# Kernel tuning notes

Measured on AMD Instinct MI355X. Metric: run time of the kernel, lower is better.

Reference implementation:

```python
import jax, jax.numpy as jnp
import numpy as np

ALPHA, GAMMA, EPS, BIG = 0.25, 2.0, 1e-7, 1e7
STRIDES = (8, 16, 32, 64, 128)
SHRINK = 0.2


def _project(boxes, fw, fh, stride):
    # shrink box around its center by SHRINK, project to feature grid (floor/ceil), clip
    cx = (boxes[..., 0] + boxes[..., 2]) * 0.5
    cy = (boxes[..., 1] + boxes[..., 3]) * 0.5
    hw = (boxes[..., 2] - boxes[..., 0]) * 0.5 * SHRINK
    hh = (boxes[..., 3] - boxes[..., 1]) * 0.5 * SHRINK
    x1 = jnp.clip(jnp.floor((cx - hw) / stride).astype(jnp.int32), 0, fw - 1)
    y1 = jnp.clip(jnp.floor((cy - hh) / stride).astype(jnp.int32), 0, fh - 1)
    x2 = jnp.clip(jnp.ceil((cx + hw) / stride).astype(jnp.int32), 1, fw)
    y2 = jnp.clip(jnp.ceil((cy + hh) / stride).astype(jnp.int32), 1, fh)
    return x1, y1, x2, y2


def _level_loss(cls_l, regr_l, boxes, labels, stride, fh, fw):
    # cls_l [B,fh,fw,C], regr_l [B,fh,fw,4], boxes [B,G,4], labels [B,G] -> loss [B,G]
    B, G = labels.shape
    x1, y1, x2, y2 = _project(boxes, fw, fh, stride)
    xs = jnp.arange(fw, dtype=jnp.int32)
    ys = jnp.arange(fh, dtype=jnp.int32)
    mx = (xs[None, None] >= x1[..., None]) & (xs[None, None] < x2[..., None])  # [B,G,fw]
    my = (ys[None, None] >= y1[..., None]) & (ys[None, None] < y2[..., None])  # [B,G,fh]
    mask = my[..., :, None] & mx[..., None, :]                                 # [B,G,fh,fw]
    denom = jnp.maximum(jnp.sum(mask, axis=(2, 3)).astype(cls_l.dtype), 1.0)   # = #positives

    # focal over one-hot(gt_label): sum_c = f0 - neg[gt] + pos[gt]
    p = jnp.clip(cls_l, EPS, 1.0 - EPS)
    neg = (1.0 - ALPHA) * p ** GAMMA * (-jnp.log1p(-p))   # per-class label=0 term
    pos = ALPHA * (1.0 - p) ** GAMMA * (-jnp.log(p))      # per-class label=1 term
    f0 = jnp.sum(neg, axis=-1)                            # [B,fh,fw]
    bidx = jnp.arange(B)[:, None]
    neg_g = neg[bidx, :, :, labels]                       # [B,G,fh,fw]
    pos_g = pos[bidx, :, :, labels]                       # [B,G,fh,fw]
    focal_map = f0[:, None] - neg_g + pos_g
    loss_cls = jnp.sum(jnp.where(mask, focal_map, 0.0), axis=(2, 3)) / denom

    # iou loss on (l,t,r,b)/(4*stride) targets, mean over region
    sx = (xs.astype(cls_l.dtype) + 0.5) * stride          # [fw]
    sy = (ys.astype(cls_l.dtype) + 0.5) * stride          # [fh]
    s = 1.0 / (4.0 * stride)
    tl = jnp.maximum(sx[None, None, None] - boxes[..., 0, None, None], 0.0) * s    # [B,G,1,fw]
    tt = jnp.maximum(sy[None, None, :, None] - boxes[..., 1, None, None], 0.0) * s  # [B,G,fh,1]
    tr = jnp.maximum(boxes[..., 2, None, None] - sx[None, None, None], 0.0) * s     # [B,G,1,fw]
    tb = jnp.maximum(boxes[..., 3, None, None] - sy[None, None, :, None], 0.0) * s  # [B,G,fh,1]
    pl = regr_l[..., 0][:, None]   # [B,1,fh,fw]
    pt = regr_l[..., 1][:, None]
    pr = regr_l[..., 2][:, None]
    pb = regr_l[..., 3][:, None]
    t_area = (tl + tr) * (tt + tb)                        # [B,G,fh,fw]
    p_area = (pl + pr) * (pt + pb)                        # [B,1,fh,fw]
    w_i = jnp.minimum(pl, tl) + jnp.minimum(pr, tr)
    h_i = jnp.minimum(pb, tb) + jnp.minimum(pt, tt)
    a_i = w_i * h_i
    a_u = t_area + p_area - a_i
    iou_map = -jnp.log((a_i + EPS) / (a_u + EPS))
    loss_iou = jnp.sum(jnp.where(mask, iou_map, 0.0), axis=(2, 3)) / denom

    empty = (x1 == x2) | (y1 == y2)                       # tf.cond 'do_not_match' branch
    return jnp.where(empty, BIG, loss_cls + loss_iou)


def _all_level_losses(cls_pred, regr_pred, gt_boxes, feature_shapes):
    fs = np.asarray(feature_shapes)
    B, C = cls_pred.shape[0], cls_pred.shape[-1]
    labels = jnp.clip(gt_boxes[..., 4].astype(jnp.int32), 0, C - 1)
    boxes = gt_boxes[..., :4]
    losses, start = [], 0
    for i, stride in enumerate(STRIDES):
        fh, fw = int(fs[i, 0]), int(fs[i, 1])
        cls_l = cls_pred[:, start:start + fh * fw].reshape(B, fh, fw, C)
        regr_l = regr_pred[:, start:start + fh * fw].reshape(B, fh, fw, 4)
        losses.append(_level_loss(cls_l, regr_l, boxes, labels, float(stride), fh, fw))
        start += fh * fw
    return jnp.stack(losses, axis=-1)   # [B,G,L]


def setup_inputs():
    key = jax.random.key(0)
    k = jax.random.split(key, 7)
    B, G, C = 8, 64, 80
    feature_shapes = np.array([[128, 128], [64, 64], [32, 32], [16, 16], [8, 8]], dtype=np.int32)
    total = int(np.prod(feature_shapes, axis=-1).sum())   # 21824 locations (1024x1024 img)
    cls_pred = jax.random.uniform(k[0], (B, total, C), jnp.float32, 0.01, 0.99)
    regr_pred = jax.random.uniform(k[1], (B, total, 4), jnp.float32, 0.05, 2.0)
    cx = jax.random.uniform(k[2], (B, G), jnp.float32, 64.0, 960.0)
    cy = jax.random.uniform(k[3], (B, G), jnp.float32, 64.0, 960.0)
    w = jax.random.uniform(k[4], (B, G), jnp.float32, 32.0, 320.0)
    h = jax.random.uniform(k[5], (B, G), jnp.float32, 32.0, 320.0)
    x1 = jnp.clip(cx - w / 2, 0.0, 1024.0)
    y1 = jnp.clip(cy - h / 2, 0.0, 1024.0)
    x2 = jnp.clip(cx + w / 2, 0.0, 1024.0)
    y2 = jnp.clip(cy + h / 2, 0.0, 1024.0)
    lbl = jax.random.randint(k[6], (B, G), 0, C).astype(jnp.float32)
    gt_boxes = jnp.stack([x1, y1, x2, y2, lbl], axis=-1)
    keep = (jnp.arange(G) < G - 16).astype(jnp.float32)   # last 16 rows are zero padding
    gt_boxes = gt_boxes * keep[None, :, None]
    return {"cls_pred": cls_pred, "regr_pred": regr_pred,
            "feature_shapes": feature_shapes, "gt_boxes": gt_boxes}


def reference(cls_pred, regr_pred, feature_shapes, gt_boxes):
    losses = _all_level_losses(cls_pred, regr_pred, gt_boxes, feature_shapes)   # [B,G,L]
    levels = jnp.argmin(losses, axis=-1).astype(jnp.int32)                      # [B,G]
    valid = jnp.sum(jnp.abs(gt_boxes[..., :4]), axis=-1) > 0                    # trim_padding_boxes
    levels = jnp.where(valid, levels, -1)                                       # padded boxes -> -1
    return levels.reshape(-1)
```

## Files before the change

kernel.cpp:

```cpp
#include <hip/hip_runtime.h>
#include <math.h>

static constexpr int B = 8;
static constexpr int G = 64;
static constexpr int C = 80;
static constexpr int TOTAL = 21824;
static constexpr float EPSF = 1e-7f;
static constexpr float BIGF = 1e7f;

static constexpr int LOCS = 128;
static constexpr int PAD  = 84;

__device__ __forceinline__ double wave_sum_d(double v) {
#pragma unroll
    for (int off = 32; off > 0; off >>= 1)
        v += __shfl_xor(v, off, 64);
    return v;
}

__device__ __forceinline__ float neg_fast(float x) {
    float p = fminf(fmaxf(x, EPSF), 1.0f - EPSF);
    float nl = -__logf(1.0f - p);
    return 0.75f * p * p * nl;
}

__global__ __launch_bounds__(128) void f0_kernel(const float* __restrict__ cls,
                                                 float* __restrict__ f0) {
    __shared__ float lds[LOCS * PAD];
    const int t = (int)threadIdx.x;
    const size_t baseLoc = (size_t)blockIdx.x * LOCS;
    const float4* gsrc = (const float4*)(cls + baseLoc * C);

#pragma unroll
    for (int r = 0; r < 20; ++r) {
        int q = r * LOCS + t;
        float4 v = gsrc[q];
        int loc = q / 20, chunk = q - loc * 20;
        *(float4*)&lds[loc * PAD + chunk * 4] = v;
    }
    __syncthreads();

    double acc = 0.0;
    const float* row = &lds[t * PAD];
#pragma unroll
    for (int i = 0; i < 20; ++i) {
        float4 v = *(const float4*)&row[i * 4];
        acc += (double)neg_fast(v.x);
        acc += (double)neg_fast(v.y);
        acc += (double)neg_fast(v.z);
        acc += (double)neg_fast(v.w);
    }
    f0[baseLoc + t] = (float)acc;
}

__global__ __launch_bounds__(320) void select_kernel(
        const float* __restrict__ cls, const float* __restrict__ regr,
        const float* __restrict__ gt, const float* __restrict__ f0,
        int* __restrict__ out) {
    const int   fws[5]     = {128, 64, 32, 16, 8};
    const int   offs[5]    = {0, 16384, 20480, 21504, 21760};
    const float strides[5] = {8.f, 16.f, 32.f, 64.f, 128.f};

    __shared__ float lloss[5];
    const int boxid = (int)blockIdx.x;
    const int l     = (int)(threadIdx.x >> 6);
    const int lane  = (int)(threadIdx.x & 63);

    const float* box = gt + (size_t)boxid * 5;
    float b0 = box[0], b1 = box[1], b2 = box[2], b3 = box[3];
    if (fabsf(b0) + fabsf(b1) + fabsf(b2) + fabsf(b3) <= 0.0f) {
        if (threadIdx.x == 0) out[boxid] = -1;
        return;
    }
    int label = (int)box[4];
    label = min(max(label, 0), C - 1);
    int b = boxid / G;

    float cx = (b0 + b2) * 0.5f, cy = (b1 + b3) * 0.5f;
    float hw = (b2 - b0) * 0.5f * 0.2f, hh = (b3 - b1) * 0.5f * 0.2f;

    const float st = strides[l];
    const int fw = fws[l];
    int x1 = min(max((int)floorf((cx - hw) / st), 0), fw - 1);
    int y1 = min(max((int)floorf((cy - hh) / st), 0), fw - 1);
    int x2 = min(max((int)ceilf((cx + hw) / st), 1), fw);
    int y2 = min(max((int)ceilf((cy + hh) / st), 1), fw);

    float loss;
    if (x1 == x2 || y1 == y2) {
        loss = BIGF;
    } else {
        int rw = x2 - x1;
        int area = rw * (y2 - y1);
        double sf = 0.0, si = 0.0;
        float s = 1.0f / (4.0f * st);
        for (int idx = lane; idx < area; idx += 64) {
            int yy = y1 + idx / rw;
            int xx = x1 + idx % rw;
            int loc = offs[l] + yy * fw + xx;
            size_t base = (size_t)b * TOTAL + (size_t)loc;
            float pv = cls[base * C + label];
            float p = fminf(fmaxf(pv, EPSF), 1.0f - EPSF);
            float neg_g = 0.75f * p * p * (-log1pf(-p));
            float omp = 1.0f - p;
            float pos_g = 0.25f * omp * omp * (-logf(p));
            sf += (double)((f0[base] - neg_g) + pos_g);
            const float4 r = *(const float4*)(regr + base * 4);
            float sx = ((float)xx + 0.5f) * st;
            float sy = ((float)yy + 0.5f) * st;
            float tl = fmaxf(sx - b0, 0.0f) * s;
            float tt = fmaxf(sy - b1, 0.0f) * s;
            float tr = fmaxf(b2 - sx, 0.0f) * s;
            float tb = fmaxf(b3 - sy, 0.0f) * s;
            float t_area = (tl + tr) * (tt + tb);
            float p_area = (r.x + r.z) * (r.y + r.w);
            float w_i = fminf(r.x, tl) + fminf(r.z, tr);
            float h_i = fminf(r.w, tb) + fminf(r.y, tt);
            float a_i = w_i * h_i;
            float a_u = (t_area + p_area) - a_i;
            si += (double)(-logf((a_i + EPSF) / (a_u + EPSF)));
        }
        sf = wave_sum_d(sf);
        si = wave_sum_d(si);
        float denom = (float)area;
        loss = (float)sf / denom + (float)si / denom;
    }
    if (lane == 0) lloss[l] = loss;
    __syncthreads();

    if (threadIdx.x == 0) {
        float best = lloss[0];
        int bestl = 0;
#pragma unroll
        for (int k = 1; k < 5; ++k) {
            float v = lloss[k];
            if (v < best) { best = v; bestl = k; }
        }
        out[boxid] = bestl;
    }
}

extern "C" void kernel_launch(void* const* d_in, const int* in_sizes, int n_in,
                              void* d_out, int out_size, void* d_ws, size_t ws_size,
                              hipStream_t stream) {
    const float* cls  = (const float*)d_in[0];
    const float* regr = (const float*)d_in[1];
    const float* gt   = (const float*)d_in[3];

    float* f0 = (float*)d_ws;

    f0_kernel<<<dim3((B * TOTAL) / LOCS), dim3(LOCS), 0, stream>>>(cls, f0);

    select_kernel<<<dim3(B * G), dim3(320), 0, stream>>>(cls, regr, gt, f0,
                                                         (int*)d_out);
}
```

Baseline: 102.6 us.

## Fuse f0 computation into select kernel, evaluating only covered locations

Removes the separate pass that computed the per-location negative-focal sum over all 80 classes for every feature location. Each select thread now computes that sum inline, only for the locations inside the shrunk box regions it visits. This avoids reading the whole class-prediction tensor, saves a kernel launch, and drops the workspace round trip. In exchange, each thread does uncoalesced 320-byte row reads and a serial 80-term loop in double precision, and locations shared by overlapping boxes get recomputed.

Measured after the change: 101.2 us. About the same (-1.3%).

```diff
diff --git a/kernel.cpp b/kernel.cpp
--- a/kernel.cpp
+++ b/kernel.cpp
@@ -7,9 +7,6 @@
 static constexpr int TOTAL = 21824;
 static constexpr float EPSF = 1e-7f;
 static constexpr float BIGF = 1e7f;
-
-static constexpr int LOCS = 128;
-static constexpr int PAD  = 84;
 
 __device__ __forceinline__ double wave_sum_d(double v) {
 #pragma unroll
@@ -24,39 +21,9 @@
     return 0.75f * p * p * nl;
 }
 
-__global__ __launch_bounds__(128) void f0_kernel(const float* __restrict__ cls,
-                                                 float* __restrict__ f0) {
-    __shared__ float lds[LOCS * PAD];
-    const int t = (int)threadIdx.x;
-    const size_t baseLoc = (size_t)blockIdx.x * LOCS;
-    const float4* gsrc = (const float4*)(cls + baseLoc * C);
-
-#pragma unroll
-    for (int r = 0; r < 20; ++r) {
-        int q = r * LOCS + t;
-        float4 v = gsrc[q];
-        int loc = q / 20, chunk = q - loc * 20;
-        *(float4*)&lds[loc * PAD + chunk * 4] = v;
-    }
-    __syncthreads();
-
-    double acc = 0.0;
-    const float* row = &lds[t * PAD];
-#pragma unroll
-    for (int i = 0; i < 20; ++i) {
-        float4 v = *(const float4*)&row[i * 4];
-        acc += (double)neg_fast(v.x);
-        acc += (double)neg_fast(v.y);
-        acc += (double)neg_fast(v.z);
-        acc += (double)neg_fast(v.w);
-    }
-    f0[baseLoc + t] = (float)acc;
-}
-
 __global__ __launch_bounds__(320) void select_kernel(
         const float* __restrict__ cls, const float* __restrict__ regr,
-        const float* __restrict__ gt, const float* __restrict__ f0,
-        int* __restrict__ out) {
+        const float* __restrict__ gt, int* __restrict__ out) {
     const int   fws[5]     = {128, 64, 32, 16, 8};
     const int   offs[5]    = {0, 16384, 20480, 21504, 21760};
     const float strides[5] = {8.f, 16.f, 32.f, 64.f, 128.f};
@@ -99,12 +66,26 @@
             int xx = x1 + idx % rw;
             int loc = offs[l] + yy * fw + xx;
             size_t base = (size_t)b * TOTAL + (size_t)loc;
+
+            const float4* crow = (const float4*)(cls + base * C);
+            double f0d = 0.0;
+#pragma unroll
+            for (int i = 0; i < 20; ++i) {
+                float4 v = crow[i];
+                f0d += (double)neg_fast(v.x);
+                f0d += (double)neg_fast(v.y);
+                f0d += (double)neg_fast(v.z);
+                f0d += (double)neg_fast(v.w);
+            }
+            float f0v = (float)f0d;
+
             float pv = cls[base * C + label];
             float p = fminf(fmaxf(pv, EPSF), 1.0f - EPSF);
             float neg_g = 0.75f * p * p * (-log1pf(-p));
             float omp = 1.0f - p;
             float pos_g = 0.25f * omp * omp * (-logf(p));
-            sf += (double)((f0[base] - neg_g) + pos_g);
+            sf += (double)((f0v - neg_g) + pos_g);
+
             const float4 r = *(const float4*)(regr + base * 4);
             float sx = ((float)xx + 0.5f) * st;
             float sy = ((float)yy + 0.5f) * st;
@@ -147,10 +128,6 @@
     const float* regr = (const float*)d_in[1];
     const float* gt   = (const float*)d_in[3];
 
-    float* f0 = (float*)d_ws;
-
-    f0_kernel<<<dim3((B * TOTAL) / LOCS), dim3(LOCS), 0, stream>>>(cls, f0);
-
-    select_kernel<<<dim3(B * G), dim3(320), 0, stream>>>(cls, regr, gt, f0,
+    select_kernel<<<dim3(B * G), dim3(320), 0, stream>>>(cls, regr, gt,
                                                          (int*)d_out);
 }
```
